# Kernel optimization log

Hardware: AMD Instinct MI355X
Metric: run time of the kernel (lower is better)

The kernel has to match this reference:

```python
import jax, jax.numpy as jnp
import numpy as np

B, T, N, K, d = 16, 64, 256, 8, 8
D = K * d
NEG = -9e15  # matches torch's -9000000000000000.0 sentinel


def _xavier(key, out_dim, in_dim):
    lim = float(np.sqrt(6.0 / (in_dim + out_dim)))
    return jax.random.uniform(key, (out_dim, in_dim), jnp.float32, -lim, lim)


def setup_inputs() -> dict:
    key = jax.random.key(0)
    ks = jax.random.split(key, 12)
    X = jax.random.normal(ks[0], (B, T, N, D), jnp.float32)
    STE = jax.random.normal(ks[1], (B, T, N, D), jnp.float32)
    W12 = _xavier(ks[2], D, 2 * D); b12 = jnp.zeros((D,), jnp.float32)
    W13 = _xavier(ks[3], D, 2 * D); b13 = jnp.zeros((D,), jnp.float32)
    W14 = _xavier(ks[4], D, 2 * D); b14 = jnp.zeros((D,), jnp.float32)
    W15 = _xavier(ks[5], D, D);     b15 = jnp.zeros((D,), jnp.float32)
    W16 = _xavier(ks[6], D, D);     b16 = jnp.zeros((D,), jnp.float32)
    return dict(X=X, STE=STE, W12=W12, b12=b12, W13=W13, b13=b13,
                W14=W14, b14=b14, W15=W15, b15=b15, W16=W16, b16=b16)


def reference(X, STE, W12, b12, W13, b13, W14, b14, W15, b15, W16, b16):
    gelu = lambda x: jax.nn.gelu(x, approximate=False)  # torch F.gelu default = erf
    Bv, Tv, Nv, Dv = X.shape
    H = jnp.concatenate([X, STE], axis=-1)              # [B,T,N,2D]
    # GELU-activated QKV projections, split into K heads of width d on last dim
    q = gelu(H @ W12.T + b12).reshape(Bv, Tv, Nv, K, d)
    k = gelu(H @ W13.T + b13).reshape(Bv, Tv, Nv, K, d)
    v = gelu(H @ W14.T + b14).reshape(Bv, Tv, Nv, K, d)
    # attention over time axis per (batch, vertex, head)
    attn = jnp.einsum('bqnkd,bsnkd->bnkqs', q, k) / jnp.sqrt(jnp.float32(d))
    causal = jnp.tril(jnp.ones((Tv, Tv), bool))         # [T,T]
    attn = jnp.where(causal, attn, jnp.float32(NEG))
    attn = jax.nn.softmax(attn, axis=-1)
    out = jnp.einsum('bnkqs,bsnkd->bqnkd', attn, v).reshape(Bv, Tv, Nv, Dv)
    # output MLP (dropout is identity in eval)
    return gelu(out @ W15.T + b15) @ W16.T + b16
```

## Files before the change

kernel.cpp:

```cpp
#include <hip/hip_runtime.h>
#include <hip/hip_bf16.h>

#define Bn 16
#define Tn 64
#define Nn 256
#define Kn 8
#define dn 8
#define Dn 64
#define TDn 128

typedef __bf16 bf16x8 __attribute__((ext_vector_type(8)));
typedef __bf16 bf16x4 __attribute__((ext_vector_type(4)));
typedef __bf16 bf16x2 __attribute__((ext_vector_type(2)));
typedef float  f32x4  __attribute__((ext_vector_type(4)));

#if __has_builtin(__builtin_amdgcn_exp2f)
#define EXP2F(x) __builtin_amdgcn_exp2f(x)
#else
#define EXP2F(x) exp2f(x)
#endif

#if __has_builtin(__builtin_amdgcn_rcpf)
#define RCPF(x) __builtin_amdgcn_rcpf(x)
#else
#define RCPF(x) (1.0f / (x))
#endif

__device__ __forceinline__ float geluf(float x) {
    const float x2 = x * x;
    const float v = x * fmaf(0.10294342f, x2, 2.30220920f);
    const float w = EXP2F(-fabsf(v));
    const float r = RCPF(1.0f + w);
    const float t = (1.0f - w) * r;
    return fmaf(0.5f * fabsf(x), t, 0.5f * x);
}

__device__ __forceinline__ bf16x8 bzero8() {
    bf16x8 z;
    #pragma unroll
    for (int e = 0; e < 8; ++e) z[e] = (__bf16)0.0f;
    return z;
}

__global__ void convert_weights(const float* __restrict__ W12, const float* __restrict__ W13,
                                const float* __restrict__ W14, const float* __restrict__ W15,
                                const float* __restrict__ W16, __bf16* __restrict__ ws)
{
    const int i = blockIdx.x * 256 + threadIdx.x;
    float v;
    if      (i < 8192)  v = W12[i];
    else if (i < 16384) v = W13[i - 8192];
    else if (i < 24576) v = W14[i - 16384];
    else if (i < 28672) v = W15[i - 24576];
    else                v = W16[i - 28672];
    ws[i] = (__bf16)v;
}

template <int J>
__device__ __forceinline__ void attn_tile(__bf16 (*qs)[72], __bf16 (*Ps)[72],
                                          bf16x8 kf0, bf16x8 kf1, bf16x8 kf2, bf16x8 kf3,
                                          bf16x8 vf0, bf16x8 vf1,
                                          int hc, int cl, int quad, int kb)
{
    bf16x8 qf = bzero8();
    if (quad == 0) qf = *reinterpret_cast<const bf16x8*>(&qs[16 * J + cl][hc]);

    const f32x4 zc = {0.f, 0.f, 0.f, 0.f};
    f32x4 st[4];
    st[0] = __builtin_amdgcn_mfma_f32_16x16x32_bf16(kf0, qf, zc, 0, 0, 0);
    if constexpr (J >= 1) st[1] = __builtin_amdgcn_mfma_f32_16x16x32_bf16(kf1, qf, zc, 0, 0, 0);
    if constexpr (J >= 2) st[2] = __builtin_amdgcn_mfma_f32_16x16x32_bf16(kf2, qf, zc, 0, 0, 0);
    if constexpr (J >= 3) st[3] = __builtin_amdgcn_mfma_f32_16x16x32_bf16(kf3, qf, zc, 0, 0, 0);

    #pragma unroll
    for (int r = 0; r < 4; ++r)
        st[J][r] = (4 * quad + r > cl) ? -3.0e38f : st[J][r];

    float mx = -3.0e38f;
    #pragma unroll
    for (int i = 0; i <= J; ++i) {
        #pragma unroll
        for (int r = 0; r < 4; ++r) mx = fmaxf(mx, st[i][r]);
    }
    mx = fmaxf(mx, __shfl_xor(mx, 16));
    mx = fmaxf(mx, __shfl_xor(mx, 32));

    float sum = 0.f;
    #pragma unroll
    for (int i = 0; i <= J; ++i) {
        #pragma unroll
        for (int r = 0; r < 4; ++r) {
            const float p = EXP2F(st[i][r] - mx);
            st[i][r] = p;
            sum += p;
        }
    }
    sum += __shfl_xor(sum, 16);
    sum += __shfl_xor(sum, 32);

    #pragma unroll
    for (int i = 0; i <= J; ++i) {
        bf16x4 pk;
        #pragma unroll
        for (int r = 0; r < 4; ++r) pk[r] = (__bf16)st[i][r];
        *reinterpret_cast<bf16x4*>(&Ps[cl][16 * i + 4 * quad]) = pk;
    }

    f32x4 o = {0.f, 0.f, 0.f, 0.f};
    {
        const bf16x8 pf = *reinterpret_cast<const bf16x8*>(&Ps[cl][kb]);
        o = __builtin_amdgcn_mfma_f32_16x16x32_bf16(vf0, pf, o, 0, 0, 0);
    }
    if constexpr (J >= 2) {
        const bf16x8 pf = *reinterpret_cast<const bf16x8*>(&Ps[cl][32 + kb]);
        o = __builtin_amdgcn_mfma_f32_16x16x32_bf16(vf1, pf, o, 0, 0, 0);
    }

    const float inv = RCPF(sum);
    if (quad < 2) {
        bf16x4 ov;
        #pragma unroll
        for (int r = 0; r < 4; ++r) ov[r] = (__bf16)(o[r] * inv);
        *reinterpret_cast<bf16x4*>(&qs[16 * J + cl][hc + 4 * quad]) = ov;
    }
}

__global__ __launch_bounds__(256, 4)
void tam_fused(const float* __restrict__ X,
               const float* __restrict__ STE,
               const float* __restrict__ b12, const float* __restrict__ b13,
               const float* __restrict__ b14, const float* __restrict__ b15,
               const float* __restrict__ b16,
               const __bf16* __restrict__ Wb,
               float* __restrict__ Out)
{
    __shared__ __align__(16) char smem[36864];
    __bf16 (*vt)[72]  = reinterpret_cast<__bf16 (*)[72]>(smem);
    __bf16 (*qs)[72]  = reinterpret_cast<__bf16 (*)[72]>(smem + 18432);
    __bf16 (*ks)[72]  = reinterpret_cast<__bf16 (*)[72]>(smem + 27648);

    const int bn   = blockIdx.x;
    const int b    = bn >> 8;
    const int n    = bn & 255;
    const int tid  = threadIdx.x;
    const int lane = tid & 63;
    const int wv   = __builtin_amdgcn_readfirstlane(tid >> 6);
    const int cl   = lane & 15;
    const int quad = lane >> 4;
    const int kb   = quad * 8;
    const int m0   = wv * 16;

    __bf16 (*Ps)[72] = reinterpret_cast<__bf16 (*)[72]>(smem + 9216 + wv * 2304);

    const __bf16* Wqkv = Wb;
    const __bf16* W15b = Wb + 24576;
    const __bf16* W16b = Wb + 28672;

    {
        bf16x8 af[4];
        {
            const int t = m0 + cl;
            const size_t rb = (((size_t)b * Tn + t) * Nn + n) * (size_t)Dn;
            const float4* Xr = reinterpret_cast<const float4*>(X + rb);
            const float4* Sr = reinterpret_cast<const float4*>(STE + rb);
            #pragma unroll
            for (int kk = 0; kk < 4; ++kk) {
                const float4* src = (kk < 2) ? Xr : Sr;
                const int fi = (kk & 1) * 8 + quad * 2;
                const float4 f0 = src[fi];
                const float4 f1 = src[fi + 1];
                bf16x8 a;
                a[0] = (__bf16)f0.x; a[1] = (__bf16)f0.y;
                a[2] = (__bf16)f0.z; a[3] = (__bf16)f0.w;
                a[4] = (__bf16)f1.x; a[5] = (__bf16)f1.y;
                a[6] = (__bf16)f1.z; a[7] = (__bf16)f1.w;
                af[kk] = a;
            }
        }

        #pragma unroll
        for (int nt = 0; nt < 12; ++nt) {
            const int n0 = nt * 16;
            f32x4 acc = {0.f, 0.f, 0.f, 0.f};
            #pragma unroll
            for (int kk = 0; kk < 4; ++kk) {
                const bf16x8 bf = *reinterpret_cast<const bf16x8*>(
                    &Wqkv[(n0 + cl) * TDn + kk * 32 + kb]);
                acc = __builtin_amdgcn_mfma_f32_16x16x32_bf16(af[kk], bf, acc, 0, 0, 0);
            }
            if (n0 < 64) {
                const float bias = b12[n0 + cl];
                #pragma unroll
                for (int r = 0; r < 4; ++r) {
                    const int row = m0 + 4 * quad + r;
                    qs[row][n0 + cl] = (__bf16)(geluf(acc[r] + bias) * 0.51006951f);
                }
            } else if (n0 < 128) {
                const float bias = b13[n0 - 64 + cl];
                #pragma unroll
                for (int r = 0; r < 4; ++r) {
                    const int row = m0 + 4 * quad + r;
                    ks[row][n0 - 64 + cl] = (__bf16)geluf(acc[r] + bias);
                }
            } else {
                const float bias = b14[n0 - 128 + cl];
                bf16x4 pv;
                #pragma unroll
                for (int r = 0; r < 4; ++r) pv[r] = (__bf16)geluf(acc[r] + bias);
                *reinterpret_cast<bf16x4*>(&vt[n0 - 128 + cl][m0 + 4 * quad]) = pv;
            }
        }
    }
    __syncthreads();

    {
        #pragma unroll
        for (int hh = 0; hh < 2; ++hh) {
            const int h  = 2 * wv + hh;
            const int hc = 8 * h;

            bf16x8 kf0 = bzero8(), kf1 = bzero8(), kf2 = bzero8(), kf3 = bzero8();
            if (quad == 0) {
                kf0 = *reinterpret_cast<const bf16x8*>(&ks[ 0 + cl][hc]);
                kf1 = *reinterpret_cast<const bf16x8*>(&ks[16 + cl][hc]);
                kf2 = *reinterpret_cast<const bf16x8*>(&ks[32 + cl][hc]);
                kf3 = *reinterpret_cast<const bf16x8*>(&ks[48 + cl][hc]);
            }
            bf16x8 vf0 = bzero8(), vf1 = bzero8();
            if (cl < 8) {
                vf0 = *reinterpret_cast<const bf16x8*>(&vt[hc + cl][kb]);
                vf1 = *reinterpret_cast<const bf16x8*>(&vt[hc + cl][32 + kb]);
            }
            *reinterpret_cast<bf16x8*>(&Ps[cl][16 * quad])     = bzero8();
            *reinterpret_cast<bf16x8*>(&Ps[cl][16 * quad + 8]) = bzero8();

            attn_tile<0>(qs, Ps, kf0, kf1, kf2, kf3, vf0, vf1, hc, cl, quad, kb);
            attn_tile<1>(qs, Ps, kf0, kf1, kf2, kf3, vf0, vf1, hc, cl, quad, kb);
            attn_tile<2>(qs, Ps, kf0, kf1, kf2, kf3, vf0, vf1, hc, cl, quad, kb);
            attn_tile<3>(qs, Ps, kf0, kf1, kf2, kf3, vf0, vf1, hc, cl, quad, kb);
        }
    }
    __syncthreads();

    {
        const bf16x8 a0 = *reinterpret_cast<const bf16x8*>(&qs[m0 + cl][kb]);
        const bf16x8 a1 = *reinterpret_cast<const bf16x8*>(&qs[m0 + cl][32 + kb]);
        #pragma unroll
        for (int nt = 0; nt < 4; ++nt) {
            const int n0 = nt * 16;
            f32x4 acc = {0.f, 0.f, 0.f, 0.f};
            const bf16x8 bf0 = *reinterpret_cast<const bf16x8*>(&W15b[(n0 + cl) * Dn + kb]);
            acc = __builtin_amdgcn_mfma_f32_16x16x32_bf16(a0, bf0, acc, 0, 0, 0);
            const bf16x8 bf1 = *reinterpret_cast<const bf16x8*>(&W15b[(n0 + cl) * Dn + 32 + kb]);
            acc = __builtin_amdgcn_mfma_f32_16x16x32_bf16(a1, bf1, acc, 0, 0, 0);
            const float bias = b15[n0 + cl];
            #pragma unroll
            for (int r = 0; r < 4; ++r) {
                const int row = m0 + 4 * quad + r;
                ks[row][n0 + cl] = (__bf16)geluf(acc[r] + bias);
            }
        }
    }

    {
        const bf16x8 a0 = *reinterpret_cast<const bf16x8*>(&ks[m0 + cl][kb]);
        const bf16x8 a1 = *reinterpret_cast<const bf16x8*>(&ks[m0 + cl][32 + kb]);
        #pragma unroll
        for (int nt = 0; nt < 4; ++nt) {
            const int n0 = nt * 16;
            f32x4 acc = {0.f, 0.f, 0.f, 0.f};
            const bf16x8 bf0 = *reinterpret_cast<const bf16x8*>(&W16b[(n0 + cl) * Dn + kb]);
            acc = __builtin_amdgcn_mfma_f32_16x16x32_bf16(a0, bf0, acc, 0, 0, 0);
            const bf16x8 bf1 = *reinterpret_cast<const bf16x8*>(&W16b[(n0 + cl) * Dn + 32 + kb]);
            acc = __builtin_amdgcn_mfma_f32_16x16x32_bf16(a1, bf1, acc, 0, 0, 0);
            const float bias = b16[n0 + cl];
            #pragma unroll
            for (int r = 0; r < 4; ++r) {
                const int row = m0 + 4 * quad + r;
                Out[((size_t)(b * Tn + row) * Nn + n) * Dn + n0 + cl] = acc[r] + bias;
            }
        }
    }
}

extern "C" void kernel_launch(void* const* d_in, const int* in_sizes, int n_in,
                              void* d_out, int out_size, void* d_ws, size_t ws_size,
                              hipStream_t stream)
{
    (void)in_sizes; (void)n_in; (void)out_size; (void)ws_size;
    const float* X   = (const float*)d_in[0];
    const float* STE = (const float*)d_in[1];
    const float* W12 = (const float*)d_in[2];
    const float* b12 = (const float*)d_in[3];
    const float* W13 = (const float*)d_in[4];
    const float* b13 = (const float*)d_in[5];
    const float* W14 = (const float*)d_in[6];
    const float* b14 = (const float*)d_in[7];
    const float* W15 = (const float*)d_in[8];
    const float* b15 = (const float*)d_in[9];
    const float* W16 = (const float*)d_in[10];
    const float* b16 = (const float*)d_in[11];
    float* Out = (float*)d_out;
    __bf16* ws = (__bf16*)d_ws;

    hipLaunchKernelGGL(convert_weights, dim3(128), dim3(256), 0, stream,
                       W12, W13, W14, W15, W16, ws);
    hipLaunchKernelGGL(tam_fused, dim3(Bn * Nn), dim3(256), 0, stream,
                       X, STE, b12, b13, b14, b15, b16, ws, Out);
}
```

Baseline: 277.6 us.

## Transpose MFMA operands for vectorized stores, shrink P scratch, raise occupancy

Swaps the MFMA A/B operands in the Q/K projection and output MLP so each lane holds four consecutive output columns. Scalar bf16 LDS stores and scalar fp32 global stores become packed bf16x4 and float4 writes. The per-wave P scratch buffer is cut to a 32-column tile, written in two halves with explicit zero padding, which drops the separate zero-fill and shrinks LDS from 36 KB to 32 KB. Launch bounds move to 5 blocks per CU, which may force register spilling.

```diff
diff --git a/kernel.cpp b/kernel.cpp
--- a/kernel.cpp
+++ b/kernel.cpp
@@ -39,6 +39,12 @@
     bf16x8 z;
     #pragma unroll
     for (int e = 0; e < 8; ++e) z[e] = (__bf16)0.0f;
+    return z;
+}
+__device__ __forceinline__ bf16x4 bzero4() {
+    bf16x4 z;
+    #pragma unroll
+    for (int e = 0; e < 4; ++e) z[e] = (__bf16)0.0f;
     return z;
 }
 
@@ -57,7 +63,7 @@
 }
 
 template <int J>
-__device__ __forceinline__ void attn_tile(__bf16 (*qs)[72], __bf16 (*Ps)[72],
+__device__ __forceinline__ void attn_tile(__bf16 (*qs)[72], __bf16 (*Ps)[40],
                                           bf16x8 kf0, bf16x8 kf1, bf16x8 kf2, bf16x8 kf3,
                                           bf16x8 vf0, bf16x8 vf1,
                                           int hc, int cl, int quad, int kb)
@@ -98,21 +104,38 @@
     sum += __shfl_xor(sum, 16);
     sum += __shfl_xor(sum, 32);
 
-    #pragma unroll
-    for (int i = 0; i <= J; ++i) {
-        bf16x4 pk;
-        #pragma unroll
-        for (int r = 0; r < 4; ++r) pk[r] = (__bf16)st[i][r];
-        *reinterpret_cast<bf16x4*>(&Ps[cl][16 * i + 4 * quad]) = pk;
-    }
-
     f32x4 o = {0.f, 0.f, 0.f, 0.f};
-    {
+
+    {
+        bf16x4 pk0;
+        #pragma unroll
+        for (int r = 0; r < 4; ++r) pk0[r] = (__bf16)st[0][r];
+        *reinterpret_cast<bf16x4*>(&Ps[cl][4 * quad]) = pk0;
+        if constexpr (J >= 1) {
+            bf16x4 pk1;
+            #pragma unroll
+            for (int r = 0; r < 4; ++r) pk1[r] = (__bf16)st[1][r];
+            *reinterpret_cast<bf16x4*>(&Ps[cl][16 + 4 * quad]) = pk1;
+        } else {
+            *reinterpret_cast<bf16x4*>(&Ps[cl][16 + 4 * quad]) = bzero4();
+        }
         const bf16x8 pf = *reinterpret_cast<const bf16x8*>(&Ps[cl][kb]);
         o = __builtin_amdgcn_mfma_f32_16x16x32_bf16(vf0, pf, o, 0, 0, 0);
     }
     if constexpr (J >= 2) {
-        const bf16x8 pf = *reinterpret_cast<const bf16x8*>(&Ps[cl][32 + kb]);
+        bf16x4 pk2;
+        #pragma unroll
+        for (int r = 0; r < 4; ++r) pk2[r] = (__bf16)st[2][r];
+        *reinterpret_cast<bf16x4*>(&Ps[cl][4 * quad]) = pk2;
+        if constexpr (J >= 3) {
+            bf16x4 pk3;
+            #pragma unroll
+            for (int r = 0; r < 4; ++r) pk3[r] = (__bf16)st[3][r];
+            *reinterpret_cast<bf16x4*>(&Ps[cl][16 + 4 * quad]) = pk3;
+        } else {
+            *reinterpret_cast<bf16x4*>(&Ps[cl][16 + 4 * quad]) = bzero4();
+        }
+        const bf16x8 pf = *reinterpret_cast<const bf16x8*>(&Ps[cl][kb]);
         o = __builtin_amdgcn_mfma_f32_16x16x32_bf16(vf1, pf, o, 0, 0, 0);
     }
 
@@ -125,7 +148,7 @@
     }
 }
 
-__global__ __launch_bounds__(256, 4)
+__global__ __launch_bounds__(256, 5)
 void tam_fused(const float* __restrict__ X,
                const float* __restrict__ STE,
                const float* __restrict__ b12, const float* __restrict__ b13,
@@ -134,10 +157,10 @@
                const __bf16* __restrict__ Wb,
                float* __restrict__ Out)
 {
-    __shared__ __align__(16) char smem[36864];
-    __bf16 (*vt)[72]  = reinterpret_cast<__bf16 (*)[72]>(smem);
-    __bf16 (*qs)[72]  = reinterpret_cast<__bf16 (*)[72]>(smem + 18432);
-    __bf16 (*ks)[72]  = reinterpret_cast<__bf16 (*)[72]>(smem + 27648);
+    __shared__ __align__(16) char smem[32768];
+    __bf16 (*vt)[72] = reinterpret_cast<__bf16 (*)[72]>(smem);
+    __bf16 (*qs)[72] = reinterpret_cast<__bf16 (*)[72]>(smem + 9216);
+    __bf16 (*ks)[72] = reinterpret_cast<__bf16 (*)[72]>(smem + 18432);
 
     const int bn   = blockIdx.x;
     const int b    = bn >> 8;
@@ -150,7 +173,7 @@
     const int kb   = quad * 8;
     const int m0   = wv * 16;
 
-    __bf16 (*Ps)[72] = reinterpret_cast<__bf16 (*)[72]>(smem + 9216 + wv * 2304);
+    __bf16 (*Ps)[40] = reinterpret_cast<__bf16 (*)[40]>(smem + 27648 + wv * 1280);
 
     const __bf16* Wqkv = Wb;
     const __bf16* W15b = Wb + 24576;
@@ -182,27 +205,37 @@
         for (int nt = 0; nt < 12; ++nt) {
             const int n0 = nt * 16;
             f32x4 acc = {0.f, 0.f, 0.f, 0.f};
-            #pragma unroll
-            for (int kk = 0; kk < 4; ++kk) {
-                const bf16x8 bf = *reinterpret_cast<const bf16x8*>(
-                    &Wqkv[(n0 + cl) * TDn + kk * 32 + kb]);
-                acc = __builtin_amdgcn_mfma_f32_16x16x32_bf16(af[kk], bf, acc, 0, 0, 0);
-            }
-            if (n0 < 64) {
-                const float bias = b12[n0 + cl];
+            if (nt < 8) {
                 #pragma unroll
-                for (int r = 0; r < 4; ++r) {
-                    const int row = m0 + 4 * quad + r;
-                    qs[row][n0 + cl] = (__bf16)(geluf(acc[r] + bias) * 0.51006951f);
+                for (int kk = 0; kk < 4; ++kk) {
+                    const bf16x8 bf = *reinterpret_cast<const bf16x8*>(
+                        &Wqkv[(n0 + cl) * TDn + kk * 32 + kb]);
+                    acc = __builtin_amdgcn_mfma_f32_16x16x32_bf16(bf, af[kk], acc, 0, 0, 0);
                 }
-            } else if (n0 < 128) {
-                const float bias = b13[n0 - 64 + cl];
-                #pragma unroll
-                for (int r = 0; r < 4; ++r) {
-                    const int row = m0 + 4 * quad + r;
-                    ks[row][n0 - 64 + cl] = (__bf16)geluf(acc[r] + bias);
+                if (nt < 4) {
+                    const float4 bs = *reinterpret_cast<const float4*>(&b12[n0 + 4 * quad]);
+                    bf16x4 pk;
+                    pk[0] = (__bf16)(geluf(acc[0] + bs.x) * 0.51006951f);
+                    pk[1] = (__bf16)(geluf(acc[1] + bs.y) * 0.51006951f);
+                    pk[2] = (__bf16)(geluf(acc[2] + bs.z) * 0.51006951f);
+                    pk[3] = (__bf16)(geluf(acc[3] + bs.w) * 0.51006951f);
+                    *reinterpret_cast<bf16x4*>(&qs[m0 + cl][n0 + 4 * quad]) = pk;
+                } else {
+                    const float4 bs = *reinterpret_cast<const float4*>(&b13[n0 - 64 + 4 * quad]);
+                    bf16x4 pk;
+                    pk[0] = (__bf16)geluf(acc[0] + bs.x);
+                    pk[1] = (__bf16)geluf(acc[1] + bs.y);
+                    pk[2] = (__bf16)geluf(acc[2] + bs.z);
+                    pk[3] = (__bf16)geluf(acc[3] + bs.w);
+                    *reinterpret_cast<bf16x4*>(&ks[m0 + cl][n0 - 64 + 4 * quad]) = pk;
                 }
             } else {
+                #pragma unroll
+                for (int kk = 0; kk < 4; ++kk) {
+                    const bf16x8 bf = *reinterpret_cast<const bf16x8*>(
+                        &Wqkv[(n0 + cl) * TDn + kk * 32 + kb]);
+                    acc = __builtin_amdgcn_mfma_f32_16x16x32_bf16(af[kk], bf, acc, 0, 0, 0);
+                }
                 const float bias = b14[n0 - 128 + cl];
                 bf16x4 pv;
                 #pragma unroll
@@ -231,8 +264,6 @@
                 vf0 = *reinterpret_cast<const bf16x8*>(&vt[hc + cl][kb]);
                 vf1 = *reinterpret_cast<const bf16x8*>(&vt[hc + cl][32 + kb]);
             }
-            *reinterpret_cast<bf16x8*>(&Ps[cl][16 * quad])     = bzero8();
-            *reinterpret_cast<bf16x8*>(&Ps[cl][16 * quad + 8]) = bzero8();
 
             attn_tile<0>(qs, Ps, kf0, kf1, kf2, kf3, vf0, vf1, hc, cl, quad, kb);
             attn_tile<1>(qs, Ps, kf0, kf1, kf2, kf3, vf0, vf1, hc, cl, quad, kb);
@@ -243,42 +274,45 @@
     __syncthreads();
 
     {
-        const bf16x8 a0 = *reinterpret_cast<const bf16x8*>(&qs[m0 + cl][kb]);
-        const bf16x8 a1 = *reinterpret_cast<const bf16x8*>(&qs[m0 + cl][32 + kb]);
+        const bf16x8 h0 = *reinterpret_cast<const bf16x8*>(&qs[m0 + cl][kb]);
+        const bf16x8 h1 = *reinterpret_cast<const bf16x8*>(&qs[m0 + cl][32 + kb]);
         #pragma unroll
         for (int nt = 0; nt < 4; ++nt) {
             const int n0 = nt * 16;
             f32x4 acc = {0.f, 0.f, 0.f, 0.f};
-            const bf16x8 bf0 = *reinterpret_cast<const bf16x8*>(&W15b[(n0 + cl) * Dn + kb]);
-            acc = __builtin_amdgcn_mfma_f32_16x16x32_bf16(a0, bf0, acc, 0, 0, 0);
-            const bf16x8 bf1 = *reinterpret_cast<const bf16x8*>(&W15b[(n0 + cl) * Dn + 32 + kb]);
-            acc = __builtin_amdgcn_mfma_f32_16x16x32_bf16(a1, bf1, acc, 0, 0, 0);
-            const float bias = b15[n0 + cl];
-            #pragma unroll
-            for (int r = 0; r < 4; ++r) {
-                const int row = m0 + 4 * quad + r;
-                ks[row][n0 + cl] = (__bf16)geluf(acc[r] + bias);
-            }
-        }
-    }
-
-    {
-        const bf16x8 a0 = *reinterpret_cast<const bf16x8*>(&ks[m0 + cl][kb]);
-        const bf16x8 a1 = *reinterpret_cast<const bf16x8*>(&ks[m0 + cl][32 + kb]);
+            const bf16x8 w0 = *reinterpret_cast<const bf16x8*>(&W15b[(n0 + cl) * Dn + kb]);
+            acc = __builtin_amdgcn_mfma_f32_16x16x32_bf16(w0, h0, acc, 0, 0, 0);
+            const bf16x8 w1 = *reinterpret_cast<const bf16x8*>(&W15b[(n0 + cl) * Dn + 32 + kb]);
+            acc = __builtin_amdgcn_mfma_f32_16x16x32_bf16(w1, h1, acc, 0, 0, 0);
+            const float4 bs = *reinterpret_cast<const float4*>(&b15[n0 + 4 * quad]);
+            bf16x4 pk;
+            pk[0] = (__bf16)geluf(acc[0] + bs.x);
+            pk[1] = (__bf16)geluf(acc[1] + bs.y);
+            pk[2] = (__bf16)geluf(acc[2] + bs.z);
+            pk[3] = (__bf16)geluf(acc[3] + bs.w);
+            *reinterpret_cast<bf16x4*>(&ks[m0 + cl][n0 + 4 * quad]) = pk;
+        }
+    }
+
+    {
+        const bf16x8 h0 = *reinterpret_cast<const bf16x8*>(&ks[m0 + cl][kb]);
+        const bf16x8 h1 = *reinterpret_cast<const bf16x8*>(&ks[m0 + cl][32 + kb]);
+        const size_t ob = (((size_t)(b * Tn + m0 + cl)) * Nn + n) * (size_t)Dn;
         #pragma unroll
         for (int nt = 0; nt < 4; ++nt) {
             const int n0 = nt * 16;
             f32x4 acc = {0.f, 0.f, 0.f, 0.f};
-            const bf16x8 bf0 = *reinterpret_cast<const bf16x8*>(&W16b[(n0 + cl) * Dn + kb]);
-            acc = __builtin_amdgcn_mfma_f32_16x16x32_bf16(a0, bf0, acc, 0, 0, 0);
-            const bf16x8 bf1 = *reinterpret_cast<const bf16x8*>(&W16b[(n0 + cl) * Dn + 32 + kb]);
-            acc = __builtin_amdgcn_mfma_f32_16x16x32_bf16(a1, bf1, acc, 0, 0, 0);
-            const float bias = b16[n0 + cl];
-            #pragma unroll
-            for (int r = 0; r < 4; ++r) {
-                const int row = m0 + 4 * quad + r;
-                Out[((size_t)(b * Tn + row) * Nn + n) * Dn + n0 + cl] = acc[r] + bias;
-            }
+            const bf16x8 w0 = *reinterpret_cast<const bf16x8*>(&W16b[(n0 + cl) * Dn + kb]);
+            acc = __builtin_amdgcn_mfma_f32_16x16x32_bf16(w0, h0, acc, 0, 0, 0);
+            const bf16x8 w1 = *reinterpret_cast<const bf16x8*>(&W16b[(n0 + cl) * Dn + 32 + kb]);
+            acc = __builtin_amdgcn_mfma_f32_16x16x32_bf16(w1, h1, acc, 0, 0, 0);
+            const float4 bs = *reinterpret_cast<const float4*>(&b16[n0 + 4 * quad]);
+            float4 ov;
+            ov.x = acc[0] + bs.x;
+            ov.y = acc[1] + bs.y;
+            ov.z = acc[2] + bs.z;
+            ov.w = acc[3] + bs.w;
+            *reinterpret_cast<float4*>(&Out[ob + n0 + 4 * quad]) = ov;
         }
     }
 }
```

Measured after the change: 282.0 us. About the same (+1.6%).
